# Optimization experiments

Measured on AMD Instinct MI355X. Metric: run time of the kernel, lower is better.

The kernel has to match this reference:

```python
import jax, jax.numpy as jnp
import numpy as np

B, N, H, HEADS, L, V, T = 4, 256, 256, 4, 128, 256, 100
FF = 4 * H

def _ln(x, g, b, eps=1e-5):
    m = jnp.mean(x, -1, keepdims=True)
    v = jnp.mean((x - m) ** 2, -1, keepdims=True)
    return (x - m) / jnp.sqrt(v + eps) * g + b

def _mha(h, w_qkv, b_qkv, w_o, b_o):
    b, n, hd = h.shape
    d = hd // HEADS
    q, k, v = jnp.split(h @ w_qkv + b_qkv, 3, axis=-1)
    q = q.reshape(b, n, HEADS, d)
    k = k.reshape(b, n, HEADS, d)
    v = v.reshape(b, n, HEADS, d)
    s = jnp.einsum('bihd,bjhd->bhij', q, k) / jnp.sqrt(jnp.float32(d))
    a = jax.nn.softmax(s, axis=-1)
    o = jnp.einsum('bhij,bjhd->bihd', a, v).reshape(b, n, hd)
    return o @ w_o + b_o

def _edge_logits(h, w1, b1, w2, b2):
    # concat([h_i, h_j], -1) @ w1 == h_i @ w1[:H] + h_j @ w1[H:]  (avoids (B,N,N,2H) materialization)
    hi = h @ w1[:H]
    hj = h @ w1[H:]
    pre = hi[:, :, None, :] + hj[:, None, :, :] + b1  # (B,N,N,H)
    return (jax.nn.gelu(pre, approximate=False) @ w2 + b2)[..., 0]

def _gnn_block(x, nbr, qw, qb, kw, kb, vw, vb, sw, sb, l1g, l1b, f1w, f1b, f2w, f2b, l2g, l2b):
    # TransformerConv (PyG, concat=True, root_weight=True) as dense masked attention over in-neighbors.
    b, n, hd = x.shape
    d = hd // HEADS
    q = (x @ qw + qb).reshape(b, n, HEADS, d)
    k = (x @ kw + kb).reshape(b, n, HEADS, d)
    v = (x @ vw + vb).reshape(b, n, HEADS, d)
    s = jnp.einsum('bihd,bjhd->bhij', q, k) / jnp.sqrt(jnp.float32(d))
    m = nbr[:, None, :, :]  # (B,1,N,N); nbr[b,i,j]=True iff edge j->i
    a = jax.nn.softmax(jnp.where(m, s, -1e30), axis=-1) * m  # no-neighbor rows aggregate to 0
    agg = jnp.einsum('bhij,bjhd->bihd', a, v).reshape(b, n, hd)
    x = _ln(x + agg + x @ sw + sb, l1g, l1b)
    ffn = jax.nn.gelu(x @ f1w + f1b, approximate=False) @ f2w + f2b
    return _ln(x + ffn, l2g, l2b)

def _forward(noisy_tokens, t, z, lp1_w, lp1_b, lp2_w, lp2_b, tok_emb, time_tab, time_w, time_b, pos_tab, enc_qkv_w, enc_qkv_b, enc_o_w, enc_o_b, enc_ln1_g, enc_ln1_b, enc_f1_w, enc_f1_b, enc_f2_w, enc_f2_b, enc_ln2_g, enc_ln2_b, gq_w, gq_b, gk_w, gk_b, gv_w, gv_b, gs_w, gs_b, g_ln1_g, g_ln1_b, g_f1_w, g_f1_b, g_f2_w, g_f2_b, g_ln2_g, g_ln2_b, nh1_w, nh1_b, nh2_w, nh2_b, eh1_w, eh1_b, eh2_w, eh2_b, sh1_w, sh1_b, sh2_w, sh2_b):
    lat = jax.nn.relu(z @ lp1_w + lp1_b) @ lp2_w + lp2_b  # (B,H)
    time_e = jax.nn.gelu(time_tab[t] @ time_w + time_b, approximate=False)  # (B,H)
    h = tok_emb[noisy_tokens] + time_e[:, None, :] + pos_tab[None, :, :] + lat[:, None, :]
    for l in range(2):  # post-norm TransformerEncoderLayer, relu FFN
        h = _ln(h + _mha(h, enc_qkv_w[l], enc_qkv_b[l], enc_o_w[l], enc_o_b[l]), enc_ln1_g[l], enc_ln1_b[l])
        h = _ln(h + jax.nn.relu(h @ enc_f1_w[l] + enc_f1_b[l]) @ enc_f2_w[l] + enc_f2_b[l], enc_ln2_g[l], enc_ln2_b[l])
    el0 = _edge_logits(h, eh1_w, eh1_b, eh2_w, eh2_b)
    nbr = jnp.swapaxes(jax.nn.sigmoid(el0) > 0.3, 1, 2)  # transpose: adj[j,i] -> in-neighbors of i
    x = h
    for l in range(4):
        x = _gnn_block(x, nbr, gq_w[l], gq_b[l], gk_w[l], gk_b[l], gv_w[l], gv_b[l], gs_w[l], gs_b[l], g_ln1_g[l], g_ln1_b[l], g_f1_w[l], g_f1_b[l], g_f2_w[l], g_f2_b[l], g_ln2_g[l], g_ln2_b[l])
    node_logits = jax.nn.gelu(x @ nh1_w + nh1_b, approximate=False) @ nh2_w + nh2_b
    edge_logits = _edge_logits(x, eh1_w, eh1_b, eh2_w, eh2_b)
    size_logits = jax.nn.relu(lat @ sh1_w + sh1_b) @ sh2_w + sh2_b
    return node_logits, edge_logits, size_logits

def setup_inputs():
    key = jax.random.key(0)
    ks = iter(jax.random.split(key, 70))
    def p(shape):
        return jax.random.normal(next(ks), shape, dtype=jnp.float32) * 0.02
    return {
        'z': jax.random.normal(next(ks), (B, L), dtype=jnp.float32),
        'noisy_tokens': jax.random.randint(next(ks), (B, N), 0, V),
        't': jax.random.randint(next(ks), (B,), 0, T),
        'lp1_w': p((L, H)), 'lp1_b': p((H,)), 'lp2_w': p((H, H)), 'lp2_b': p((H,)),
        'tok_emb': p((V, H)), 'time_tab': p((T, H)), 'time_w': p((H, H)), 'time_b': p((H,)),
        'pos_tab': p((N, H)),
        'enc_qkv_w': p((2, H, 3 * H)), 'enc_qkv_b': p((2, 3 * H)),
        'enc_o_w': p((2, H, H)), 'enc_o_b': p((2, H)),
        'enc_ln1_g': jnp.ones((2, H)), 'enc_ln1_b': jnp.zeros((2, H)),
        'enc_f1_w': p((2, H, FF)), 'enc_f1_b': p((2, FF)),
        'enc_f2_w': p((2, FF, H)), 'enc_f2_b': p((2, H)),
        'enc_ln2_g': jnp.ones((2, H)), 'enc_ln2_b': jnp.zeros((2, H)),
        'gq_w': p((4, H, H)), 'gq_b': p((4, H)),
        'gk_w': p((4, H, H)), 'gk_b': p((4, H)),
        'gv_w': p((4, H, H)), 'gv_b': p((4, H)),
        'gs_w': p((4, H, H)), 'gs_b': p((4, H)),
        'g_ln1_g': jnp.ones((4, H)), 'g_ln1_b': jnp.zeros((4, H)),
        'g_f1_w': p((4, H, FF)), 'g_f1_b': p((4, FF)),
        'g_f2_w': p((4, FF, H)), 'g_f2_b': p((4, H)),
        'g_ln2_g': jnp.ones((4, H)), 'g_ln2_b': jnp.zeros((4, H)),
        'nh1_w': p((H, H)), 'nh1_b': p((H,)),
        'nh2_w': p((H, V)), 'nh2_b': p((V,)),
        'eh1_w': p((2 * H, H)), 'eh1_b': p((H,)),
        'eh2_w': p((H, 1)), 'eh2_b': p((1,)),
        'sh1_w': p((H, H // 2)), 'sh1_b': p((H // 2,)),
        'sh2_w': p((H // 2, N)), 'sh2_b': p((N,)),
    }

def reference(z, noisy_tokens, t, lp1_w, lp1_b, lp2_w, lp2_b, tok_emb, time_tab, time_w, time_b, pos_tab, enc_qkv_w, enc_qkv_b, enc_o_w, enc_o_b, enc_ln1_g, enc_ln1_b, enc_f1_w, enc_f1_b, enc_f2_w, enc_f2_b, enc_ln2_g, enc_ln2_b, gq_w, gq_b, gk_w, gk_b, gv_w, gv_b, gs_w, gs_b, g_ln1_g, g_ln1_b, g_f1_w, g_f1_b, g_f2_w, g_f2_b, g_ln2_g, g_ln2_b, nh1_w, nh1_b, nh2_w, nh2_b, eh1_w, eh1_b, eh2_w, eh2_b, sh1_w, sh1_b, sh2_w, sh2_b):
    return _forward(noisy_tokens, t, z, lp1_w, lp1_b, lp2_w, lp2_b, tok_emb, time_tab, time_w, time_b, pos_tab, enc_qkv_w, enc_qkv_b, enc_o_w, enc_o_b, enc_ln1_g, enc_ln1_b, enc_f1_w, enc_f1_b, enc_f2_w, enc_f2_b, enc_ln2_g, enc_ln2_b, gq_w, gq_b, gk_w, gk_b, gv_w, gv_b, gs_w, gs_b, g_ln1_g, g_ln1_b, g_f1_w, g_f1_b, g_f2_w, g_f2_b, g_ln2_g, g_ln2_b, nh1_w, nh1_b, nh2_w, nh2_b, eh1_w, eh1_b, eh2_w, eh2_b, sh1_w, sh1_b, sh2_w, sh2_b)
```

## Files before the change

kernel.cpp:

```cpp
#include <hip/hip_runtime.h>
#include <math.h>


typedef __attribute__((ext_vector_type(8))) short bf16x8;
typedef __attribute__((ext_vector_type(4))) float f32x4;

__device__ __forceinline__ unsigned short f2b(float f) {
    unsigned u = __float_as_uint(f);
    u += 0x7FFFu + ((u >> 16) & 1u);
    return (unsigned short)(u >> 16);
}
__device__ __forceinline__ unsigned pack2(float a, float b) {
    return (unsigned)f2b(a) | ((unsigned)f2b(b) << 16);
}
__device__ __forceinline__ bf16x8 as_frag(uint4 v) {
    union { uint4 u; bf16x8 f; } x; x.u = v; return x.f;
}
__device__ __forceinline__ bf16x8 ld_frag_f32(const float* p) {
    const float4 v0 = *(const float4*)p;
    const float4 v1 = *(const float4*)(p + 4);
    union { unsigned u[4]; bf16x8 f; } x;
    x.u[0] = pack2(v0.x, v0.y); x.u[1] = pack2(v0.z, v0.w);
    x.u[2] = pack2(v1.x, v1.y); x.u[3] = pack2(v1.z, v1.w);
    return x.f;
}

__device__ __forceinline__ float gelu_f(float x) {
    const float y  = 0.70710678118654752f * x;
    const float ay = fabsf(y);
    const float t  = __builtin_amdgcn_rcpf(fmaf(0.3275911f, ay, 1.0f));
    float S = fmaf(t, 1.061405429f, -1.453152027f);
    S = fmaf(t, S, 1.421413741f);
    S = fmaf(t, S, -0.284496736f);
    S = fmaf(t, S, 0.254829592f);
    S = S * t;
    const float e = __expf(-ay * ay);
    const float E = fmaf(-S, e, 1.0f);
    return 0.5f * x * (1.0f + copysignf(E, y));
}

struct PrepEnt { const float* src; unsigned dstOff; int K; int N; unsigned tstart; };
struct PrepTab { int n; PrepEnt e[36]; };

__global__ __launch_bounds__(256) void k_prep(PrepTab tab, unsigned short* __restrict__ wt)
{
    const int bx = blockIdx.x;
    int ei = 0;
    for (int i = 0; i < tab.n; ++i) if (tab.e[i].tstart <= (unsigned)bx) ei = i;
    const PrepEnt E = tab.e[ei];
    const int tIdx = bx - E.tstart;
    const int ntn = E.N >> 6;
    const int kt = tIdx / ntn, nt = tIdx % ntn;
    const int tid = threadIdx.x;
    __shared__ unsigned Tl[64][36];
    {
        const int r = tid >> 2, c = (tid & 3) * 16;
        const float* s = E.src + (size_t)(kt * 64 + r) * E.N + nt * 64 + c;
        unsigned o[8];
        #pragma unroll
        for (int q = 0; q < 4; ++q) {
            const float4 v = *(const float4*)(s + q * 4);
            o[q * 2 + 0] = pack2(v.x, v.y);
            o[q * 2 + 1] = pack2(v.z, v.w);
        }
        *(uint4*)&Tl[r][c / 2 + 0] = make_uint4(o[0], o[1], o[2], o[3]);
        *(uint4*)&Tl[r][c / 2 + 4] = make_uint4(o[4], o[5], o[6], o[7]);
    }
    __syncthreads();
    {
        const int rn = tid >> 2, ck = (tid & 3) * 16;
        const int sh = (rn & 1) * 16, hw = rn >> 1;
        unsigned o[8];
        #pragma unroll
        for (int s = 0; s < 8; ++s) {
            const unsigned lo = (Tl[ck + 2 * s][hw] >> sh) & 0xFFFFu;
            const unsigned hi = (Tl[ck + 2 * s + 1][hw] >> sh) & 0xFFFFu;
            o[s] = lo | (hi << 16);
        }
        unsigned short* d = wt + E.dstOff + (size_t)(nt * 64 + rn) * E.K + kt * 64 + ck;
        *(uint4*)(d + 0) = make_uint4(o[0], o[1], o[2], o[3]);
        *(uint4*)(d + 8) = make_uint4(o[4], o[5], o[6], o[7]);
    }
}


__device__ __forceinline__ void gd64_body(
    const float* __restrict__ A, const unsigned short* __restrict__ Wt,
    const float* __restrict__ bias, float* __restrict__ C,
    int K, int ldc, int act, int m0, int n0)
{
    const int tid = threadIdx.x;
    const int l = tid & 63, wid = tid >> 6;
    const int wm = wid & 1, wn = wid >> 1, lr = l & 15, lg = l >> 4;
    const float* a0 = A + (size_t)(m0 + wm * 32 + lr) * K + lg * 8;
    const float* a1 = a0 + (size_t)16 * K;
    const unsigned short* b0 = Wt + (size_t)(n0 + wn * 32 + lr) * K + lg * 8;
    const unsigned short* b1 = b0 + (size_t)16 * K;
    f32x4 acc00 = {0.f,0.f,0.f,0.f}, acc01 = acc00, acc10 = acc00, acc11 = acc00;
    #pragma unroll 2
    for (int k0 = 0; k0 < K; k0 += 32) {
        const bf16x8 fa0 = ld_frag_f32(a0 + k0);
        const bf16x8 fa1 = ld_frag_f32(a1 + k0);
        const bf16x8 fb0 = as_frag(*(const uint4*)(b0 + k0));
        const bf16x8 fb1 = as_frag(*(const uint4*)(b1 + k0));
        acc00 = __builtin_amdgcn_mfma_f32_16x16x32_bf16(fa0, fb0, acc00, 0, 0, 0);
        acc01 = __builtin_amdgcn_mfma_f32_16x16x32_bf16(fa0, fb1, acc01, 0, 0, 0);
        acc10 = __builtin_amdgcn_mfma_f32_16x16x32_bf16(fa1, fb0, acc10, 0, 0, 0);
        acc11 = __builtin_amdgcn_mfma_f32_16x16x32_bf16(fa1, fb1, acc11, 0, 0, 0);
    }
    const int cb0 = n0 + wn * 32 + lr, cb1 = cb0 + 16;
    const float bv0 = bias ? bias[cb0] : 0.f;
    const float bv1 = bias ? bias[cb1] : 0.f;
    #pragma unroll
    for (int r = 0; r < 4; ++r) {
        const int row0 = m0 + wm * 32 + lg * 4 + r;
        const int row1 = row0 + 16;
        float v00 = acc00[r] + bv0, v01 = acc01[r] + bv1;
        float v10 = acc10[r] + bv0, v11 = acc11[r] + bv1;
        if (act == 1) {
            v00 = fmaxf(v00, 0.f); v01 = fmaxf(v01, 0.f);
            v10 = fmaxf(v10, 0.f); v11 = fmaxf(v11, 0.f);
        } else if (act == 2) {
            v00 = gelu_f(v00); v01 = gelu_f(v01);
            v10 = gelu_f(v10); v11 = gelu_f(v11);
        }
        C[(size_t)row0 * ldc + cb0] = v00;
        C[(size_t)row0 * ldc + cb1] = v01;
        C[(size_t)row1 * ldc + cb0] = v10;
        C[(size_t)row1 * ldc + cb1] = v11;
    }
}

__global__ __launch_bounds__(256) void k_gd64(
    const float* __restrict__ A, const unsigned short* __restrict__ Wt,
    const float* __restrict__ bias, float* __restrict__ C, int K, int ldc, int act)
{
    gd64_body(A, Wt, bias, C, K, ldc, act, blockIdx.y * 64, blockIdx.x * 64);
}

__device__ __forceinline__ void gd32_body(
    const float* __restrict__ A, const unsigned short* __restrict__ Wt,
    const float* __restrict__ bias, float* __restrict__ C,
    int K, int ldc, int act, int m0, int n0)
{
    const int tid = threadIdx.x;
    const int l = tid & 63, wid = tid >> 6;
    const int qm = wid & 1, qn = wid >> 1, lr = l & 15, lg = l >> 4;
    const float* ap = A + (size_t)(m0 + qm * 16 + lr) * K + lg * 8;
    const unsigned short* bp = Wt + (size_t)(n0 + qn * 16 + lr) * K + lg * 8;
    f32x4 acc = {0.f,0.f,0.f,0.f};
    #pragma unroll 4
    for (int k0 = 0; k0 < K; k0 += 32) {
        const bf16x8 fa = ld_frag_f32(ap + k0);
        const bf16x8 fb = as_frag(*(const uint4*)(bp + k0));
        acc = __builtin_amdgcn_mfma_f32_16x16x32_bf16(fa, fb, acc, 0, 0, 0);
    }
    const int cc = n0 + qn * 16 + lr;
    const float bv = bias ? bias[cc] : 0.f;
    #pragma unroll
    for (int r = 0; r < 4; ++r) {
        const int row = m0 + qm * 16 + lg * 4 + r;
        float v = acc[r] + bv;
        if (act == 1) v = fmaxf(v, 0.f); else if (act == 2) v = gelu_f(v);
        C[(size_t)row * ldc + cc] = v;
    }
}

__global__ __launch_bounds__(256) void k_gd32(
    const float* __restrict__ A, const unsigned short* __restrict__ Wt,
    const float* __restrict__ bias, float* __restrict__ C, int K, int ldc, int act)
{
    gd32_body(A, Wt, bias, C, K, ldc, act, blockIdx.y * 32, blockIdx.x * 32);
}

struct MW4 { const unsigned short* wt[4]; const float* b[4]; };
__global__ __launch_bounds__(256) void k_gd32_4(
    const float* __restrict__ A, MW4 p, float* __restrict__ C)
{
    const int z = blockIdx.z;
    gd32_body(A, p.wt[z], p.b[z], C + z * 256, 256, 1024, 0,
              blockIdx.y * 32, blockIdx.x * 32);
}

__global__ __launch_bounds__(256) void k_mv(
    const float* __restrict__ A, const int* __restrict__ aidx, int K,
    const float* __restrict__ W, const float* __restrict__ bias,
    float* __restrict__ out, int N, int act)
{
    const int r = blockIdx.x, c0 = blockIdx.y * 64;
    const int c = threadIdx.x & 63, ks = threadIdx.x >> 6;
    const float* arow = A + (size_t)(aidx ? aidx[r] : r) * K;
    float s = 0.f;
    for (int k = ks; k < K; k += 4) s += arow[k] * W[(size_t)k * N + c0 + c];
    __shared__ float red[4][64];
    red[ks][c] = s;
    __syncthreads();
    if (ks == 0) {
        float v = red[0][c] + red[1][c] + red[2][c] + red[3][c] + (bias ? bias[c0 + c] : 0.f);
        if (act == 1) v = fmaxf(v, 0.f); else if (act == 2) v = gelu_f(v);
        out[(size_t)r * N + c0 + c] = v;
    }
}

__global__ __launch_bounds__(256) void k_embed(
    const int* __restrict__ tok, const float* __restrict__ tok_emb,
    const float* __restrict__ pos, const float* __restrict__ lat,
    const float* __restrict__ te, float* __restrict__ h)
{
    const int r = blockIdx.x, c = threadIdx.x;
    const int b = r >> 8, n = r & 255;
    h[(size_t)r * 256 + c] = tok_emb[(size_t)tok[r] * 256 + c] + te[b * 256 + c]
                           + pos[n * 256 + c] + lat[b * 256 + c];
}

__global__ __launch_bounds__(256) void k_attn2(
    const float* __restrict__ qkv, int ld, int qo, int ko, int vo,
    const unsigned char* __restrict__ mask, float* __restrict__ out)
{
    const int blk = blockIdx.x;
    const int ig = blk & 15, hh = (blk >> 4) & 3, b = blk >> 6;
    const int i0 = ig * 16;
    const int t = threadIdx.x;
    __shared__ float Qs[16][68];
    __shared__ float Ts[64][68];
    __shared__ float Ss[16][260];

    {
        const int r = t >> 4, c = (t & 15) * 4;
        *(float4*)&Qs[r][c] = *(const float4*)&qkv[(size_t)(b * 256 + i0 + r) * ld + qo + hh * 64 + c];
    }
    const int i = t >> 4, tx = t & 15;

    for (int jt = 0; jt < 4; ++jt) {
        __syncthreads();
        {
            const int jr = t >> 2, cs = (t & 3) * 16;
            const float* src = &qkv[(size_t)(b * 256 + jt * 64 + jr) * ld + ko + hh * 64 + cs];
            *(float4*)&Ts[jr][cs + 0]  = *(const float4*)(src + 0);
            *(float4*)&Ts[jr][cs + 4]  = *(const float4*)(src + 4);
            *(float4*)&Ts[jr][cs + 8]  = *(const float4*)(src + 8);
            *(float4*)&Ts[jr][cs + 12] = *(const float4*)(src + 12);
        }
        __syncthreads();
        float s0 = 0.f, s1 = 0.f, s2 = 0.f, s3 = 0.f;
        #pragma unroll 8
        for (int d = 0; d < 64; ++d) {
            const float qd = Qs[i][d];
            s0 += qd * Ts[tx][d];
            s1 += qd * Ts[tx + 16][d];
            s2 += qd * Ts[tx + 32][d];
            s3 += qd * Ts[tx + 48][d];
        }
        Ss[i][jt * 64 + tx]      = s0;
        Ss[i][jt * 64 + tx + 16] = s1;
        Ss[i][jt * 64 + tx + 32] = s2;
        Ss[i][jt * 64 + tx + 48] = s3;
    }

    {
        const unsigned char* mrow = mask ? &mask[(size_t)(b * 256 + i0 + i) * 256] : nullptr;
        float sv[16]; bool okv[16];
        float m = -3.0e38f;
        #pragma unroll
        for (int k = 0; k < 16; ++k) {
            const int j = tx + 16 * k;
            const float s = Ss[i][j] * 0.125f;
            const bool ok = mrow ? (mrow[j] != 0) : true;
            sv[k] = s; okv[k] = ok;
            if (ok) m = fmaxf(m, s);
        }
        #pragma unroll
        for (int w = 1; w < 16; w <<= 1) m = fmaxf(m, __shfl_xor(m, w, 64));
        float ev[16]; float sum = 0.f;
        #pragma unroll
        for (int k = 0; k < 16; ++k) {
            ev[k] = okv[k] ? __expf(sv[k] - m) : 0.f;
            sum += ev[k];
        }
        #pragma unroll
        for (int w = 1; w < 16; w <<= 1) sum += __shfl_xor(sum, w, 64);
        const float inv = (sum > 0.f) ? 1.f / sum : 0.f;
        #pragma unroll
        for (int k = 0; k < 16; ++k) Ss[i][tx + 16 * k] = ev[k] * inv;
    }

    const int d4 = tx * 4;
    float4 o = {0.f, 0.f, 0.f, 0.f};
    for (int jt = 0; jt < 4; ++jt) {
        __syncthreads();
        {
            const int jr = t >> 2, cs = (t & 3) * 16;
            const float* src = &qkv[(size_t)(b * 256 + jt * 64 + jr) * ld + vo + hh * 64 + cs];
            *(float4*)&Ts[jr][cs + 0]  = *(const float4*)(src + 0);
            *(float4*)&Ts[jr][cs + 4]  = *(const float4*)(src + 4);
            *(float4*)&Ts[jr][cs + 8]  = *(const float4*)(src + 8);
            *(float4*)&Ts[jr][cs + 12] = *(const float4*)(src + 12);
        }
        __syncthreads();
        #pragma unroll 8
        for (int j = 0; j < 64; ++j) {
            const float p = Ss[i][jt * 64 + j];
            const float4 v4 = *(const float4*)&Ts[j][d4];
            o.x += p * v4.x; o.y += p * v4.y; o.z += p * v4.z; o.w += p * v4.w;
        }
    }
    *(float4*)&out[(size_t)(b * 256 + i0 + i) * 256 + hh * 64 + d4] = o;
}

__global__ __launch_bounds__(256) void k_ln2(
    const float* __restrict__ a, const float* __restrict__ bb, int ldb,
    const float* __restrict__ cc, int ldc,
    const float* __restrict__ g, const float* __restrict__ beta, float* __restrict__ out)
{
    const int r = blockIdx.x * 4 + (threadIdx.x >> 6);
    const int c4 = (threadIdx.x & 63) * 4;
    float4 v = *(const float4*)&a[(size_t)r * 256 + c4];
    if (bb) {
        const float4 u = *(const float4*)&bb[(size_t)r * ldb + c4];
        v.x += u.x; v.y += u.y; v.z += u.z; v.w += u.w;
    }
    if (cc) {
        const float4 u = *(const float4*)&cc[(size_t)r * ldc + c4];
        v.x += u.x; v.y += u.y; v.z += u.z; v.w += u.w;
    }
    float s = v.x + v.y + v.z + v.w;
    float q = v.x * v.x + v.y * v.y + v.z * v.z + v.w * v.w;
    #pragma unroll
    for (int w = 1; w < 64; w <<= 1) {
        s += __shfl_xor(s, w, 64);
        q += __shfl_xor(q, w, 64);
    }
    const float mean = s * (1.0f / 256.0f);
    const float var  = q * (1.0f / 256.0f) - mean * mean;
    const float inv  = rsqrtf(var + 1e-5f);
    const float4 gg = *(const float4*)&g[c4];
    const float4 be = *(const float4*)&beta[c4];
    float4 o;
    o.x = (v.x - mean) * inv * gg.x + be.x;
    o.y = (v.y - mean) * inv * gg.y + be.y;
    o.z = (v.z - mean) * inv * gg.z + be.z;
    o.w = (v.w - mean) * inv * gg.w + be.w;
    *(float4*)&out[(size_t)r * 256 + c4] = o;
}

__global__ __launch_bounds__(256) void k_edge3(
    const float* __restrict__ hi, const float* __restrict__ hj,
    const float* __restrict__ w2, const float* __restrict__ b2,
    float* __restrict__ val_out, unsigned char* __restrict__ mask_out)
{
    const int jg = blockIdx.x, ig = blockIdx.y, b = blockIdx.z;
    const int t = threadIdx.x;
    __shared__ float his[16][268];
    __shared__ float hjs[16][268];
    __shared__ float w2s[256];
    {
        const int r = t >> 4, c = (t & 15) * 16;
        const float* s1 = &hi[(size_t)(b * 256 + ig * 16 + r) * 256 + c];
        const float* s2 = &hj[(size_t)(b * 256 + jg * 16 + r) * 256 + c];
        #pragma unroll
        for (int q = 0; q < 4; ++q) {
            *(float4*)&his[r][c + q * 4] = *(const float4*)(s1 + q * 4);
            *(float4*)&hjs[r][c + q * 4] = *(const float4*)(s2 + q * 4);
        }
        w2s[t] = w2[t];
    }
    __syncthreads();
    const int i = t >> 4, j = t & 15;
    float acc = 0.f;
    #pragma unroll 4
    for (int h4 = 0; h4 < 64; ++h4) {
        const float4 hv  = *(const float4*)&hjs[j][h4 * 4];
        const float4 hi4 = *(const float4*)&his[i][h4 * 4];
        const float4 w4  = *(const float4*)&w2s[h4 * 4];
        acc += gelu_f(hi4.x + hv.x) * w4.x;
        acc += gelu_f(hi4.y + hv.y) * w4.y;
        acc += gelu_f(hi4.z + hv.z) * w4.z;
        acc += gelu_f(hi4.w + hv.w) * w4.w;
    }
    const float v = acc + b2[0];
    if (val_out)  val_out[(size_t)b * 65536 + (ig * 16 + i) * 256 + jg * 16 + j] = v;
    if (mask_out) mask_out[(size_t)b * 65536 + (jg * 16 + j) * 256 + ig * 16 + i] =
                      (v > -0.84729786038720f) ? 1 : 0;
}

extern "C" void kernel_launch(void* const* d_in, const int* in_sizes, int n_in,
                              void* d_out, int out_size, void* d_ws, size_t ws_size,
                              hipStream_t stream) {
    const float* z     = (const float*)d_in[0];
    const int*   tok   = (const int*)d_in[1];
    const int*   tt    = (const int*)d_in[2];
    const float* lp1w  = (const float*)d_in[3];
    const float* lp1b  = (const float*)d_in[4];
    const float* lp2w  = (const float*)d_in[5];
    const float* lp2b  = (const float*)d_in[6];
    const float* temb  = (const float*)d_in[7];
    const float* ttab  = (const float*)d_in[8];
    const float* tw    = (const float*)d_in[9];
    const float* tb    = (const float*)d_in[10];
    const float* pos   = (const float*)d_in[11];
    const float* qkvw  = (const float*)d_in[12];
    const float* qkvb  = (const float*)d_in[13];
    const float* ow    = (const float*)d_in[14];
    const float* ob    = (const float*)d_in[15];
    const float* ln1g  = (const float*)d_in[16];
    const float* ln1b  = (const float*)d_in[17];
    const float* f1w   = (const float*)d_in[18];
    const float* f1b   = (const float*)d_in[19];
    const float* f2w   = (const float*)d_in[20];
    const float* f2b   = (const float*)d_in[21];
    const float* ln2g  = (const float*)d_in[22];
    const float* ln2b  = (const float*)d_in[23];
    const float* gqw   = (const float*)d_in[24];
    const float* gqb   = (const float*)d_in[25];
    const float* gkw   = (const float*)d_in[26];
    const float* gkb   = (const float*)d_in[27];
    const float* gvw   = (const float*)d_in[28];
    const float* gvb   = (const float*)d_in[29];
    const float* gsw   = (const float*)d_in[30];
    const float* gsb   = (const float*)d_in[31];
    const float* gl1g  = (const float*)d_in[32];
    const float* gl1b  = (const float*)d_in[33];
    const float* gf1w  = (const float*)d_in[34];
    const float* gf1b  = (const float*)d_in[35];
    const float* gf2w  = (const float*)d_in[36];
    const float* gf2b  = (const float*)d_in[37];
    const float* gl2g  = (const float*)d_in[38];
    const float* gl2b  = (const float*)d_in[39];
    const float* nh1w  = (const float*)d_in[40];
    const float* nh1b  = (const float*)d_in[41];
    const float* nh2w  = (const float*)d_in[42];
    const float* nh2b  = (const float*)d_in[43];
    const float* eh1w  = (const float*)d_in[44];
    const float* eh1b  = (const float*)d_in[45];
    const float* eh2w  = (const float*)d_in[46];
    const float* eh2b  = (const float*)d_in[47];
    const float* sh1w  = (const float*)d_in[48];
    const float* sh1b  = (const float*)d_in[49];
    const float* sh2w  = (const float*)d_in[50];
    const float* sh2b  = (const float*)d_in[51];

    float* W = (float*)d_ws;
    float* Hh  = W + 0;
    float* QK  = W + 262144;
    float* AO  = W + 1310720;
    float* T1  = W + 1572864;
    float* HI  = W + 1835008;
    float* HJ  = W + 2097152;
    float* LAT = W + 2359296;
    float* TE  = W + 2360320;
    float* A1  = W + 2361344;
    float* SH  = W + 2362368;
    unsigned char* MASK = (unsigned char*)(W + 2362880);
    unsigned short* wt  = (unsigned short*)(W + 2428416);

    float* out      = (float*)d_out;
    float* out_node = out;
    float* out_edge = out + 262144;
    float* out_sz   = out + 524288;

    PrepTab tab; int ne = 0; unsigned tiles = 0;
    auto add = [&](const float* src, int K, int N, unsigned off) {
        tab.e[ne].src = src; tab.e[ne].K = K; tab.e[ne].N = N;
        tab.e[ne].dstOff = off; tab.e[ne].tstart = tiles;
        tiles += (unsigned)((K >> 6) * (N >> 6)); ++ne;
    };
    for (int l = 0; l < 2; ++l) add(qkvw + (size_t)l * 196608, 256, 768,  0 + l * 196608);
    for (int l = 0; l < 2; ++l) add(ow   + (size_t)l * 65536,  256, 256,  393216 + l * 65536);
    for (int l = 0; l < 2; ++l) add(f1w  + (size_t)l * 262144, 256, 1024, 524288 + l * 262144);
    for (int l = 0; l < 2; ++l) add(f2w  + (size_t)l * 262144, 1024, 256, 1048576 + l * 262144);
    for (int l = 0; l < 4; ++l) add(gqw  + (size_t)l * 65536,  256, 256,  1572864 + l * 65536);
    for (int l = 0; l < 4; ++l) add(gkw  + (size_t)l * 65536,  256, 256,  1835008 + l * 65536);
    for (int l = 0; l < 4; ++l) add(gvw  + (size_t)l * 65536,  256, 256,  2097152 + l * 65536);
    for (int l = 0; l < 4; ++l) add(gsw  + (size_t)l * 65536,  256, 256,  2359296 + l * 65536);
    for (int l = 0; l < 4; ++l) add(gf1w + (size_t)l * 262144, 256, 1024, 2621440 + l * 262144);
    for (int l = 0; l < 4; ++l) add(gf2w + (size_t)l * 262144, 1024, 256, 3670016 + l * 262144);
    add(nh1w, 256, 256, 4718592);
    add(nh2w, 256, 256, 4784128);
    add(eh1w,         256, 256, 4849664);
    add(eh1w + 65536, 256, 256, 4915200);
    tab.n = ne;
    k_prep<<<tiles, 256, 0, stream>>>(tab, wt);

    auto g64 = [&](const float* Aa, size_t wtoff, const float* bias, float* Cc,
                   int N, int K, int ldc, int act) {
        k_gd64<<<dim3(N / 64, 16), 256, 0, stream>>>(Aa, wt + wtoff, bias, Cc, K, ldc, act);
    };
    auto g32 = [&](const float* Aa, size_t wtoff, const float* bias, float* Cc,
                   int K, int ldc, int act) {
        k_gd32<<<dim3(8, 32), 256, 0, stream>>>(Aa, wt + wtoff, bias, Cc, K, ldc, act);
    };

    k_mv<<<dim3(4, 4), 256, 0, stream>>>(z,    nullptr, 128, lp1w, lp1b, A1,     256, 1);
    k_mv<<<dim3(4, 4), 256, 0, stream>>>(ttab, tt,      256, tw,   tb,   TE,     256, 2);
    k_mv<<<dim3(4, 4), 256, 0, stream>>>(A1,   nullptr, 256, lp2w, lp2b, LAT,    256, 0);
    k_mv<<<dim3(4, 2), 256, 0, stream>>>(LAT,  nullptr, 256, sh1w, sh1b, SH,     128, 1);
    k_mv<<<dim3(4, 4), 256, 0, stream>>>(SH,   nullptr, 128, sh2w, sh2b, out_sz, 256, 0);

    k_embed<<<1024, 256, 0, stream>>>(tok, temb, pos, LAT, TE, Hh);

    for (int l = 0; l < 2; ++l) {
        g64(Hh, (size_t)l * 196608, qkvb + l * 768, QK, 768, 256, 768, 0);
        k_attn2<<<256, 256, 0, stream>>>(QK, 768, 0, 256, 512, nullptr, AO);
        g32(AO, 393216 + (size_t)l * 65536, ob + l * 256, T1, 256, 256, 0);
        k_ln2<<<256, 256, 0, stream>>>(Hh, T1, 256, nullptr, 0, ln1g + l * 256, ln1b + l * 256, Hh);
        g64(Hh, 524288 + (size_t)l * 262144, f1b + l * 1024, QK, 1024, 256, 1024, 1);
        g32(QK, 1048576 + (size_t)l * 262144, f2b + l * 256, T1, 1024, 256, 0);
        k_ln2<<<256, 256, 0, stream>>>(Hh, T1, 256, nullptr, 0, ln2g + l * 256, ln2b + l * 256, Hh);
    }

    g32(Hh, 4849664, eh1b, HI, 256, 256, 0);
    g32(Hh, 4915200, nullptr, HJ, 256, 256, 0);
    k_edge3<<<dim3(16, 16, 4), 256, 0, stream>>>(HI, HJ, eh2w, eh2b, nullptr, MASK);

    for (int l = 0; l < 4; ++l) {
        MW4 p;
        p.wt[0] = wt + 1572864 + (size_t)l * 65536; p.b[0] = gqb + l * 256;
        p.wt[1] = wt + 1835008 + (size_t)l * 65536; p.b[1] = gkb + l * 256;
        p.wt[2] = wt + 2097152 + (size_t)l * 65536; p.b[2] = gvb + l * 256;
        p.wt[3] = wt + 2359296 + (size_t)l * 65536; p.b[3] = gsb + l * 256;
        k_gd32_4<<<dim3(8, 32, 4), 256, 0, stream>>>(Hh, p, QK);
        k_attn2<<<256, 256, 0, stream>>>(QK, 1024, 0, 256, 512, MASK, AO);
        k_ln2<<<256, 256, 0, stream>>>(Hh, AO, 256, QK + 768, 1024, gl1g + l * 256, gl1b + l * 256, Hh);
        g64(Hh, 2621440 + (size_t)l * 262144, gf1b + l * 1024, QK, 1024, 256, 1024, 2);
        g32(QK, 3670016 + (size_t)l * 262144, gf2b + l * 256, T1, 1024, 256, 0);
        k_ln2<<<256, 256, 0, stream>>>(Hh, T1, 256, nullptr, 0, gl2g + l * 256, gl2b + l * 256, Hh);
    }

    g32(Hh, 4718592, nh1b, T1, 256, 256, 2);
    g32(T1, 4784128, nh2b, out_node, 256, 256, 0);
    g32(Hh, 4849664, eh1b, HI, 256, 256, 0);
    g32(Hh, 4915200, nullptr, HJ, 256, 256, 0);
    k_edge3<<<dim3(16, 16, 4), 256, 0, stream>>>(HI, HJ, eh2w, eh2b, out_edge, nullptr);
}
```

Baseline: 750.0 us.

## Fuse output GEMMs with residual LayerNorm and batch small head GEMMs

Adds a k_gemm_ln kernel that computes a full 256-column GEMM row block per wave, adds bias and one or two residuals, and applies LayerNorm in registers. This replaces separate GEMM and LayerNorm launches in the encoder and GNN layers, dropping the intermediate write and read of T1. Independent GEMMs (edge hi/hj, node head, q/k/v) are also batched into one launch through a z-indexed parameter struct. The trade-off is that the fused kernel runs only 16 blocks with long serial MFMA chains per wave, which leaves most compute units idle.

Result: slower. 1.703 ms (+127.1%).

```diff
diff --git a/kernel.cpp b/kernel.cpp
--- a/kernel.cpp
+++ b/kernel.cpp
@@ -166,20 +166,77 @@
     }
 }
 
-__global__ __launch_bounds__(256) void k_gd32(
+struct GBe { const unsigned short* wt; const float* bias; float* C; int ldc; int act; };
+struct GB3 { GBe e[3]; };
+__global__ __launch_bounds__(256) void k_gd32b(
+    const float* __restrict__ A, GB3 p, int K)
+{
+    const GBe E = p.e[blockIdx.z];
+    gd32_body(A, E.wt, E.bias, E.C, K, E.ldc, E.act, blockIdx.y * 32, blockIdx.x * 32);
+}
+
+__global__ __launch_bounds__(256) void k_gemm_ln(
     const float* __restrict__ A, const unsigned short* __restrict__ Wt,
-    const float* __restrict__ bias, float* __restrict__ C, int K, int ldc, int act)
-{
-    gd32_body(A, Wt, bias, C, K, ldc, act, blockIdx.y * 32, blockIdx.x * 32);
-}
-
-struct MW4 { const unsigned short* wt[4]; const float* b[4]; };
-__global__ __launch_bounds__(256) void k_gd32_4(
-    const float* __restrict__ A, MW4 p, float* __restrict__ C)
-{
-    const int z = blockIdx.z;
-    gd32_body(A, p.wt[z], p.b[z], C + z * 256, 256, 1024, 0,
-              blockIdx.y * 32, blockIdx.x * 32);
+    const float* __restrict__ bias,
+    const float* __restrict__ res1, const float* __restrict__ res2, int ldr2,
+    const float* __restrict__ g, const float* __restrict__ beta,
+    float* __restrict__ outp, int K)
+{
+    const int w = threadIdx.x >> 6, l = threadIdx.x & 63;
+    const int lr = l & 15, lg = l >> 4;
+    const int r0 = blockIdx.x * 64 + w * 16;
+    const float* ap = A + (size_t)(r0 + lr) * K + lg * 8;
+    const unsigned short* bp = Wt + (size_t)lr * K + lg * 8;
+    f32x4 acc[16];
+    #pragma unroll
+    for (int nt = 0; nt < 16; ++nt) acc[nt] = (f32x4){0.f, 0.f, 0.f, 0.f};
+    for (int k0 = 0; k0 < K; k0 += 32) {
+        const bf16x8 fa = ld_frag_f32(ap + k0);
+        #pragma unroll
+        for (int nt = 0; nt < 16; ++nt) {
+            const bf16x8 fb = as_frag(*(const uint4*)(bp + (size_t)nt * 16 * K + k0));
+            acc[nt] = __builtin_amdgcn_mfma_f32_16x16x32_bf16(fa, fb, acc[nt], 0, 0, 0);
+        }
+    }
+    float sum[4] = {0.f,0.f,0.f,0.f}, sq[4] = {0.f,0.f,0.f,0.f};
+    #pragma unroll
+    for (int nt = 0; nt < 16; ++nt) {
+        const int col = nt * 16 + lr;
+        const float bv = bias ? bias[col] : 0.f;
+        #pragma unroll
+        for (int r = 0; r < 4; ++r) {
+            const int row = r0 + lg * 4 + r;
+            float v = acc[nt][r] + bv + res1[(size_t)row * 256 + col];
+            if (res2) v += res2[(size_t)row * ldr2 + col];
+            acc[nt][r] = v;
+            sum[r] += v; sq[r] += v * v;
+        }
+    }
+    #pragma unroll
+    for (int m = 1; m < 16; m <<= 1) {
+        #pragma unroll
+        for (int r = 0; r < 4; ++r) {
+            sum[r] += __shfl_xor(sum[r], m, 64);
+            sq[r]  += __shfl_xor(sq[r],  m, 64);
+        }
+    }
+    float mean[4], inv[4];
+    #pragma unroll
+    for (int r = 0; r < 4; ++r) {
+        mean[r] = sum[r] * (1.0f / 256.0f);
+        const float var = sq[r] * (1.0f / 256.0f) - mean[r] * mean[r];
+        inv[r] = rsqrtf(var + 1e-5f);
+    }
+    #pragma unroll
+    for (int nt = 0; nt < 16; ++nt) {
+        const int col = nt * 16 + lr;
+        const float gg = g[col], bb = beta[col];
+        #pragma unroll
+        for (int r = 0; r < 4; ++r) {
+            const int row = r0 + lg * 4 + r;
+            outp[(size_t)row * 256 + col] = (acc[nt][r] - mean[r]) * inv[r] * gg + bb;
+        }
+    }
 }
 
 __global__ __launch_bounds__(256) void k_mv(
@@ -305,42 +362,6 @@
         }
     }
     *(float4*)&out[(size_t)(b * 256 + i0 + i) * 256 + hh * 64 + d4] = o;
-}
-
-__global__ __launch_bounds__(256) void k_ln2(
-    const float* __restrict__ a, const float* __restrict__ bb, int ldb,
-    const float* __restrict__ cc, int ldc,
-    const float* __restrict__ g, const float* __restrict__ beta, float* __restrict__ out)
-{
-    const int r = blockIdx.x * 4 + (threadIdx.x >> 6);
-    const int c4 = (threadIdx.x & 63) * 4;
-    float4 v = *(const float4*)&a[(size_t)r * 256 + c4];
-    if (bb) {
-        const float4 u = *(const float4*)&bb[(size_t)r * ldb + c4];
-        v.x += u.x; v.y += u.y; v.z += u.z; v.w += u.w;
-    }
-    if (cc) {
-        const float4 u = *(const float4*)&cc[(size_t)r * ldc + c4];
-        v.x += u.x; v.y += u.y; v.z += u.z; v.w += u.w;
-    }
-    float s = v.x + v.y + v.z + v.w;
-    float q = v.x * v.x + v.y * v.y + v.z * v.z + v.w * v.w;
-    #pragma unroll
-    for (int w = 1; w < 64; w <<= 1) {
-        s += __shfl_xor(s, w, 64);
-        q += __shfl_xor(q, w, 64);
-    }
-    const float mean = s * (1.0f / 256.0f);
-    const float var  = q * (1.0f / 256.0f) - mean * mean;
-    const float inv  = rsqrtf(var + 1e-5f);
-    const float4 gg = *(const float4*)&g[c4];
-    const float4 be = *(const float4*)&beta[c4];
-    float4 o;
-    o.x = (v.x - mean) * inv * gg.x + be.x;
-    o.y = (v.y - mean) * inv * gg.y + be.y;
-    o.z = (v.z - mean) * inv * gg.z + be.z;
-    o.w = (v.w - mean) * inv * gg.w + be.w;
-    *(float4*)&out[(size_t)r * 256 + c4] = o;
 }
 
 __global__ __launch_bounds__(256) void k_edge3(
@@ -485,9 +506,10 @@
                    int N, int K, int ldc, int act) {
         k_gd64<<<dim3(N / 64, 16), 256, 0, stream>>>(Aa, wt + wtoff, bias, Cc, K, ldc, act);
     };
-    auto g32 = [&](const float* Aa, size_t wtoff, const float* bias, float* Cc,
-                   int K, int ldc, int act) {
-        k_gd32<<<dim3(8, 32), 256, 0, stream>>>(Aa, wt + wtoff, bias, Cc, K, ldc, act);
+    auto gln = [&](const float* Aa, size_t wtoff, const float* bias,
+                   const float* r1, const float* r2, int ldr2,
+                   const float* gg, const float* bb, float* o, int K) {
+        k_gemm_ln<<<16, 256, 0, stream>>>(Aa, wt + wtoff, bias, r1, r2, ldr2, gg, bb, o, K);
     };
 
     k_mv<<<dim3(4, 4), 256, 0, stream>>>(z,    nullptr, 128, lp1w, lp1b, A1,     256, 1);
@@ -501,34 +523,48 @@
     for (int l = 0; l < 2; ++l) {
         g64(Hh, (size_t)l * 196608, qkvb + l * 768, QK, 768, 256, 768, 0);
         k_attn2<<<256, 256, 0, stream>>>(QK, 768, 0, 256, 512, nullptr, AO);
-        g32(AO, 393216 + (size_t)l * 65536, ob + l * 256, T1, 256, 256, 0);
-        k_ln2<<<256, 256, 0, stream>>>(Hh, T1, 256, nullptr, 0, ln1g + l * 256, ln1b + l * 256, Hh);
+        gln(AO, 393216 + (size_t)l * 65536, ob + l * 256, Hh, nullptr, 0,
+            ln1g + l * 256, ln1b + l * 256, Hh, 256);
         g64(Hh, 524288 + (size_t)l * 262144, f1b + l * 1024, QK, 1024, 256, 1024, 1);
-        g32(QK, 1048576 + (size_t)l * 262144, f2b + l * 256, T1, 1024, 256, 0);
-        k_ln2<<<256, 256, 0, stream>>>(Hh, T1, 256, nullptr, 0, ln2g + l * 256, ln2b + l * 256, Hh);
-    }
-
-    g32(Hh, 4849664, eh1b, HI, 256, 256, 0);
-    g32(Hh, 4915200, nullptr, HJ, 256, 256, 0);
+        gln(QK, 1048576 + (size_t)l * 262144, f2b + l * 256, Hh, nullptr, 0,
+            ln2g + l * 256, ln2b + l * 256, Hh, 1024);
+    }
+
+    {
+        GB3 p;
+        p.e[0] = { wt + 4849664, eh1b,    HI, 256, 0 };
+        p.e[1] = { wt + 4915200, nullptr, HJ, 256, 0 };
+        p.e[2] = p.e[0];
+        k_gd32b<<<dim3(8, 32, 2), 256, 0, stream>>>(Hh, p, 256);
+    }
     k_edge3<<<dim3(16, 16, 4), 256, 0, stream>>>(HI, HJ, eh2w, eh2b, nullptr, MASK);
 
     for (int l = 0; l < 4; ++l) {
-        MW4 p;
-        p.wt[0] = wt + 1572864 + (size_t)l * 65536; p.b[0] = gqb + l * 256;
-        p.wt[1] = wt + 1835008 + (size_t)l * 65536; p.b[1] = gkb + l * 256;
-        p.wt[2] = wt + 2097152 + (size_t)l * 65536; p.b[2] = gvb + l * 256;
-        p.wt[3] = wt + 2359296 + (size_t)l * 65536; p.b[3] = gsb + l * 256;
-        k_gd32_4<<<dim3(8, 32, 4), 256, 0, stream>>>(Hh, p, QK);
+        GB3 p;
+        p.e[0] = { wt + 1572864 + (size_t)l * 65536, gqb + l * 256, QK + 0,   1024, 0 };
+        p.e[1] = { wt + 1835008 + (size_t)l * 65536, gkb + l * 256, QK + 256, 1024, 0 };
+        p.e[2] = { wt + 2097152 + (size_t)l * 65536, gvb + l * 256, QK + 512, 1024, 0 };
+        k_gd32b<<<dim3(8, 32, 3), 256, 0, stream>>>(Hh, p, 256);
         k_attn2<<<256, 256, 0, stream>>>(QK, 1024, 0, 256, 512, MASK, AO);
-        k_ln2<<<256, 256, 0, stream>>>(Hh, AO, 256, QK + 768, 1024, gl1g + l * 256, gl1b + l * 256, Hh);
+        gln(Hh, 2359296 + (size_t)l * 65536, gsb + l * 256, Hh, AO, 256,
+            gl1g + l * 256, gl1b + l * 256, Hh, 256);
         g64(Hh, 2621440 + (size_t)l * 262144, gf1b + l * 1024, QK, 1024, 256, 1024, 2);
-        g32(QK, 3670016 + (size_t)l * 262144, gf2b + l * 256, T1, 1024, 256, 0);
-        k_ln2<<<256, 256, 0, stream>>>(Hh, T1, 256, nullptr, 0, gl2g + l * 256, gl2b + l * 256, Hh);
-    }
-
-    g32(Hh, 4718592, nh1b, T1, 256, 256, 2);
-    g32(T1, 4784128, nh2b, out_node, 256, 256, 0);
-    g32(Hh, 4849664, eh1b, HI, 256, 256, 0);
-    g32(Hh, 4915200, nullptr, HJ, 256, 256, 0);
+        gln(QK, 3670016 + (size_t)l * 262144, gf2b + l * 256, Hh, nullptr, 0,
+            gl2g + l * 256, gl2b + l * 256, Hh, 1024);
+    }
+
+    {
+        GB3 p;
+        p.e[0] = { wt + 4718592, nh1b,    T1, 256, 2 };
+        p.e[1] = { wt + 4849664, eh1b,    HI, 256, 0 };
+        p.e[2] = { wt + 4915200, nullptr, HJ, 256, 0 };
+        k_gd32b<<<dim3(8, 32, 3), 256, 0, stream>>>(Hh, p, 256);
+    }
+    {
+        GB3 p;
+        p.e[0] = { wt + 4784128, nh2b, out_node, 256, 0 };
+        p.e[1] = p.e[0]; p.e[2] = p.e[0];
+        k_gd32b<<<dim3(8, 32, 1), 256, 0, stream>>>(T1, p, 256);
+    }
     k_edge3<<<dim3(16, 16, 4), 256, 0, stream>>>(HI, HJ, eh2w, eh2b, out_edge, nullptr);
 }
```
